# Kernel optimization log

Measured on AMD Instinct MI355X. Metric: run time of the kernel, lower is better.

The kernel has to match this reference:

```python
import math
import jax, jax.numpy as jnp
import numpy as np

NUM_FILTERS = 4
MAX_RADIUS = 0.999
B, L = 32, 524288


def setup_inputs() -> dict:
    key = jax.random.key(0)
    kx, kr, ka, kb1, kb2 = jax.random.split(key, 5)
    return {
        "x": jax.random.normal(kx, (B, L), dtype=jnp.float32),
        "log_radius": jax.random.normal(kr, (NUM_FILTERS,), dtype=jnp.float32),
        "raw_angle": jax.random.normal(ka, (NUM_FILTERS,), dtype=jnp.float32),
        "b0": jnp.ones((NUM_FILTERS,), dtype=jnp.float32),
        "b1": 0.1 * jax.random.normal(kb1, (NUM_FILTERS,), dtype=jnp.float32),
        "b2": 0.1 * jax.random.normal(kb2, (NUM_FILTERS,), dtype=jnp.float32),
    }


def _apply_single_biquad(x, b0, b1, b2, a1, a2):
    # Direct Form II Transposed, sequential over time via lax.scan.
    # x: (B, L); scalars b0,b1,b2,a1,a2.
    Bv = x.shape[0]
    s0 = (jnp.zeros((Bv,), x.dtype), jnp.zeros((Bv,), x.dtype))

    def step(carry, xn):
        s1, s2 = carry
        yn = b0 * xn + s1
        s1n = b1 * xn - a1 * yn + s2
        s2n = b2 * xn - a2 * yn
        return (s1n, s2n), yn

    _, ys = jax.lax.scan(step, s0, x.T)  # ys: (L, B)
    return ys.T


def reference(x, log_radius, raw_angle, b0, b1, b2):
    # Stable pole parameterization: radius in (0, MAX_RADIUS), angle in (0, pi)
    radius = jax.nn.sigmoid(log_radius) * MAX_RADIUS
    angle = jax.nn.sigmoid(raw_angle) * math.pi
    a1 = -2.0 * radius * jnp.cos(angle)  # (F,)
    a2 = radius * radius                 # (F,)
    y = x
    for f in range(NUM_FILTERS):  # cascade (series) application
        y = _apply_single_biquad(y, b0[f], b1[f], b2[f], a1[f], a2[f])
    return y
```

## Files before the change

kernel.cpp:

```cpp
#include <hip/hip_runtime.h>
#include <math.h>

#define Bn 32
#define Ln 524288
#define NF 4

#define TPB   256
#define NW    (TPB / 64)
#define CPT   18
#define OUT   4096
#define WU    512
#define S_WG  (OUT + WU)
#define TPR   (Ln / OUT)
#define NTILE 2
#define NT    (Bn * TPR / NTILE)

#define SLOT4  (S_WG / 4)
#define OSLOT4 (OUT / 4)
#define WSLOT4 (WU / 4)

#define COEF_OFF 0
#define POWJ_OFF 64
#define XW1_OFF  448
#define PLM4_OFF 512
#define WSEQ_OFF 3072

#define WAGG_L (SLOT4 * 4)
#define LDS_F  (WAGG_L + 32)

__device__ __forceinline__ constexpr int prow(int p) {
    return (p < 2) ? 0 : (p < 4) ? 1 : (p < 8) ? 2 : (p < 12) ? 3
         : (p < 18) ? 4 : (p < 24) ? 5 : (p < 32) ? 6 : 7;
}
__device__ __forceinline__ constexpr int pcol(int p) {
    return p - ((p < 2) ? 0 : (p < 4) ? 2 : (p < 8) ? 4 : (p < 12) ? 8
              : (p < 18) ? 12 : (p < 24) ? 18 : (p < 32) ? 24 : 32);
}

__global__ void precompute_k(const float* __restrict__ lr,
                             const float* __restrict__ ra,
                             const float* __restrict__ b0,
                             const float* __restrict__ b1,
                             const float* __restrict__ b2,
                             float* __restrict__ ws) {
    __shared__ double A2d[6][64];
    __shared__ float  A2f[6][64];
    __shared__ double Tw[64];
    const int t = threadIdx.x;

    if (t < NF) {
        double r   = 0.999 / (1.0 + exp(-(double)lr[t]));
        double ang = 3.14159265358979323846 / (1.0 + exp(-(double)ra[t]));
        ws[COEF_OFF + t * 5 + 0] = b0[t];
        ws[COEF_OFF + t * 5 + 1] = b1[t];
        ws[COEF_OFF + t * 5 + 2] = b2[t];
        ws[COEF_OFF + t * 5 + 3] = (float)(-2.0 * r * cos(ang));
        ws[COEF_OFF + t * 5 + 4] = (float)(r * r);
    }
    __syncthreads();

    if (t < 8) {
        double cb0[NF], cb1[NF], cb2[NF], ca1[NF], ca2[NF];
        for (int f = 0; f < NF; ++f) {
            cb0[f] = (double)ws[COEF_OFF + f * 5 + 0];
            cb1[f] = (double)ws[COEF_OFF + f * 5 + 1];
            cb2[f] = (double)ws[COEF_OFF + f * 5 + 2];
            ca1[f] = (double)ws[COEF_OFF + f * 5 + 3];
            ca2[f] = (double)ws[COEF_OFF + f * 5 + 4];
        }
        double s[8];
        for (int r = 0; r < 8; ++r) s[r] = 0.0;
        s[t] = 1.0;
        for (int n = 0; n < CPT; ++n) {
            double v = 0.0;
            for (int f = 0; f < NF; ++f) {
                double y     = cb0[f] * v + s[2 * f];
                s[2 * f]     = cb1[f] * v - ca1[f] * y + s[2 * f + 1];
                s[2 * f + 1] = cb2[f] * v - ca2[f] * y;
                v = y;
            }
            ws[WSEQ_OFF + n * 8 + t] = (float)v;
        }
        for (int r = 0; r < 8; ++r) A2d[0][r * 8 + t] = s[r];
    }
    __syncthreads();

    A2f[0][t] = (float)A2d[0][t];
    ws[POWJ_OFF + t] = A2f[0][t];
    const int r8 = t >> 3, c8 = t & 7;
    for (int j = 1; j <= 6; ++j) {
        const double* S = A2d[j - 1];
        double acc = 0.0;
        for (int m = 0; m < 8; ++m) acc += S[r8 * 8 + m] * S[m * 8 + c8];
        Tw[t] = acc;
        __syncthreads();
        if (j <= 5) {
            A2d[j][t] = Tw[t];
            A2f[j][t] = (float)Tw[t];
            ws[POWJ_OFF + j * 64 + t] = (float)Tw[t];
        } else {
            ws[XW1_OFF + t] = (float)Tw[t];
        }
        __syncthreads();
    }

    float M[64];
#pragma unroll
    for (int i = 0; i < 64; ++i) M[i] = ((i >> 3) == (i & 7)) ? 1.f : 0.f;
    for (int j = 0; j < 6; ++j) {
        if ((t >> j) & 1) {
            float Tn[64];
            for (int r = 0; r < 8; ++r)
                for (int c = 0; c < 8; ++c) {
                    float acc = 0.f;
                    for (int m = 0; m < 8; ++m)
                        acc = fmaf(M[r * 8 + m], A2f[j][m * 8 + c], acc);
                    Tn[r * 8 + c] = acc;
                }
            for (int i = 0; i < 64; ++i) M[i] = Tn[i];
        }
    }
    for (int p = 0; p < 40; ++p)
        ws[PLM4_OFF + (p >> 2) * 256 + t * 4 + (p & 3)] = M[prow(p) * 8 + pcol(p)];
}

__device__ __forceinline__ void step1(float& u, float* s,
                                      const float* c0, const float* c1,
                                      const float* c2, const float* A1,
                                      const float* A2) {
#pragma unroll
    for (int f = 0; f < NF; ++f) {
        float yv     = fmaf(c0[f], u, s[2 * f]);
        s[2 * f]     = fmaf(-A1[f], yv, fmaf(c1[f], u, s[2 * f + 1]));
        s[2 * f + 1] = fmaf(-A2[f], yv, c2[f] * u);
        u = yv;
    }
}

__device__ __forceinline__ void matvec_acc_sp(float* o, const float* __restrict__ T,
                                              const float* p) {
#pragma unroll
    for (int r = 0; r < 8; ++r) {
        const int ncol = (r | 1) + 1;
#pragma unroll
        for (int c = 0; c < 8; ++c)
            if (c < ncol) o[r] = fmaf(T[r * 8 + c], p[c], o[r]);
    }
}
__device__ __forceinline__ void matvec_rep_sp(float* h, const float* __restrict__ T) {
    float tmp[8];
#pragma unroll
    for (int r = 0; r < 8; ++r) {
        const int ncol = (r | 1) + 1;
        float acc = 0.f;
#pragma unroll
        for (int c = 0; c < 8; ++c)
            if (c < ncol) acc = fmaf(T[r * 8 + c], h[c], acc);
        tmp[r] = acc;
    }
#pragma unroll
    for (int r = 0; r < 8; ++r) h[r] = tmp[r];
}

__global__ __launch_bounds__(TPB, 8) void biquad_k(const float* __restrict__ x,
                                                   const float* __restrict__ ws,
                                                   float* __restrict__ y) {
    __shared__ __align__(16) float ldsf[LDS_F];
    float4* lds4 = (float4*)ldsf;
    float2* lds2 = (float2*)ldsf;
    const int t    = threadIdx.x;
    const int lane = t & 63;
    const int w    = t >> 6;

    const float* __restrict__ mats = ws + POWJ_OFF;
    const float* __restrict__ xw1  = ws + XW1_OFF;
    const float4* xg4 = (const float4*)x;
    float4* yg4 = (float4*)y;

    float c0[NF], c1[NF], c2[NF], A1[NF], A2[NF];
#pragma unroll
    for (int f = 0; f < NF; ++f) {
        c0[f] = ws[COEF_OFF + f * 5 + 0];
        c1[f] = ws[COEF_OFF + f * 5 + 1];
        c2[f] = ws[COEF_OFF + f * 5 + 2];
        A1[f] = ws[COEF_OFF + f * 5 + 3];
        A2[f] = ws[COEF_OFF + f * 5 + 4];
    }

    float4 pf[5];
    {
        const int tile = blockIdx.x * NTILE;
        const int tpos = tile % TPR;
        const long base4 = (long)(tile / TPR) * (Ln / 4) + (long)tpos * OSLOT4 - WSLOT4;
#pragma unroll
        for (int j = 0; j < 5; ++j) {
            const int n4 = j * TPB + t;
            pf[j] = make_float4(0.f, 0.f, 0.f, 0.f);
            if (n4 < SLOT4 && (tpos > 0 || n4 >= WSLOT4)) pf[j] = xg4[base4 + n4];
        }
    }

#pragma unroll
    for (int k = 0; k < NTILE; ++k) {
        const int tile = blockIdx.x * NTILE + k;
        const int row  = tile / TPR;
        const int tpos = tile % TPR;

        if (k > 0) __syncthreads();

#pragma unroll
        for (int j = 0; j < 5; ++j) {
            const int n4 = j * TPB + t;
            if (n4 < SLOT4) lds4[n4] = pf[j];
        }
        __syncthreads();

        if (k + 1 < NTILE) {
            const int ntile = tile + 1;
            const int ntpos = ntile % TPR;
            const long nbase4 = (long)(ntile / TPR) * (Ln / 4) + (long)ntpos * OSLOT4 - WSLOT4;
#pragma unroll
            for (int j = 0; j < 5; ++j) {
                const int n4 = j * TPB + t;
                float4 v = make_float4(0.f, 0.f, 0.f, 0.f);
                if (n4 < SLOT4 && (ntpos > 0 || n4 >= WSLOT4)) v = xg4[nbase4 + n4];
                pf[j] = v;
            }
        }

        float s[8];
#pragma unroll
        for (int r = 0; r < 8; ++r) s[r] = 0.f;
        {
            float2 xr[CPT / 2];
#pragma unroll
            for (int i = 0; i < CPT / 2; ++i) xr[i] = lds2[(CPT / 2) * t + i];
#pragma unroll
            for (int i = 0; i < CPT / 2; ++i) {
                float u;
                u = xr[i].x; step1(u, s, c0, c1, c2, A1, A2); xr[i].x = u;
                u = xr[i].y; step1(u, s, c0, c1, c2, A1, A2); xr[i].y = u;
            }
#pragma unroll
            for (int i = 0; i < CPT / 2; ++i) lds2[(CPT / 2) * t + i] = xr[i];
        }

        float v8[8];
#pragma unroll
        for (int r = 0; r < 8; ++r) v8[r] = s[r];
#pragma unroll
        for (int j = 0; j < 6; ++j) {
            const int st = 1 << j;
            float p[8];
#pragma unroll
            for (int r = 0; r < 8; ++r) p[r] = __shfl_up(v8[r], st, 64);
            if (lane >= st) matvec_acc_sp(v8, mats + j * 64, p);
        }

        if (lane == 63) {
#pragma unroll
            for (int r = 0; r < 8; ++r) ldsf[WAGG_L + w * 8 + r] = v8[r];
        }
        __syncthreads();

        float H[8];
#pragma unroll
        for (int r = 0; r < 8; ++r) H[r] = 0.f;
#pragma unroll
        for (int m = 0; m < NW - 1; ++m) {
            if (m < w) {
                matvec_rep_sp(H, xw1);
#pragma unroll
                for (int r = 0; r < 8; ++r) H[r] += ldsf[WAGG_L + m * 8 + r];
            }
        }

        float dlt[8];
#pragma unroll
        for (int r = 0; r < 8; ++r) dlt[r] = 0.f;
        {
            const float4* plm4 = (const float4*)(ws + PLM4_OFF);
#pragma unroll
            for (int g = 0; g < 10; ++g) {
                const float4 mv = plm4[g * 64 + lane];
                dlt[prow(4 * g + 0)] = fmaf(mv.x, H[pcol(4 * g + 0)], dlt[prow(4 * g + 0)]);
                dlt[prow(4 * g + 1)] = fmaf(mv.y, H[pcol(4 * g + 1)], dlt[prow(4 * g + 1)]);
                dlt[prow(4 * g + 2)] = fmaf(mv.z, H[pcol(4 * g + 2)], dlt[prow(4 * g + 2)]);
                dlt[prow(4 * g + 3)] = fmaf(mv.w, H[pcol(4 * g + 3)], dlt[prow(4 * g + 3)]);
            }
        }
#pragma unroll
        for (int r = 0; r < 8; ++r) {
            const float pv = __shfl_up(v8[r], 1, 64);
            if (lane > 0) dlt[r] += pv;
        }

        const float* __restrict__ wsq = ws + WSEQ_OFF;
#pragma unroll
        for (int i = 0; i < CPT / 2; ++i) {
            float2 v = lds2[(CPT / 2) * t + i];
            float a0 = 0.f, a1 = 0.f;
#pragma unroll
            for (int kk = 0; kk < 8; ++kk) {
                a0 = fmaf(wsq[(2 * i) * 8 + kk], dlt[kk], a0);
                a1 = fmaf(wsq[(2 * i + 1) * 8 + kk], dlt[kk], a1);
            }
            v.x += a0;
            v.y += a1;
            lds2[(CPT / 2) * t + i] = v;
        }
        __syncthreads();

        const long obase4 = (long)row * (Ln / 4) + (long)tpos * OSLOT4;
#pragma unroll
        for (int j = 0; j < 4; ++j) {
            const int n4 = WSLOT4 + j * TPB + t;
            yg4[obase4 + (n4 - WSLOT4)] = lds4[n4];
        }
    }
}

extern "C" void kernel_launch(void* const* d_in, const int* in_sizes, int n_in,
                              void* d_out, int out_size, void* d_ws, size_t ws_size,
                              hipStream_t stream) {
    const float* x  = (const float*)d_in[0];
    const float* lr = (const float*)d_in[1];
    const float* ra = (const float*)d_in[2];
    const float* b0 = (const float*)d_in[3];
    const float* b1 = (const float*)d_in[4];
    const float* b2 = (const float*)d_in[5];
    float* y  = (float*)d_out;
    float* ws = (float*)d_ws;

    precompute_k<<<dim3(1), dim3(64), 0, stream>>>(lr, ra, b0, b1, b2, ws);
    biquad_k<<<dim3(NT), dim3(TPB), 0, stream>>>(x, ws, y);
}
```

Measured before the change: 56.99 us.

## Double-buffer input tiles in LDS via direct global-to-LDS loads

```diff
diff --git a/kernel.cpp b/kernel.cpp
--- a/kernel.cpp
+++ b/kernel.cpp
@@ -12,8 +12,8 @@
 #define WU    512
 #define S_WG  (OUT + WU)
 #define TPR   (Ln / OUT)
-#define NTILE 2
-#define NT    (Bn * TPR / NTILE)
+#define NTILE 4
+#define NWG   (Bn * TPR / NTILE)
 
 #define SLOT4  (S_WG / 4)
 #define OSLOT4 (OUT / 4)
@@ -24,9 +24,6 @@
 #define XW1_OFF  448
 #define PLM4_OFF 512
 #define WSEQ_OFF 3072
-
-#define WAGG_L (SLOT4 * 4)
-#define LDS_F  (WAGG_L + 32)
 
 __device__ __forceinline__ constexpr int prow(int p) {
     return (p < 2) ? 0 : (p < 4) ? 1 : (p < 8) ? 2 : (p < 12) ? 3
@@ -162,20 +159,35 @@
     for (int r = 0; r < 8; ++r) h[r] = tmp[r];
 }
 
-__global__ __launch_bounds__(TPB, 8) void biquad_k(const float* __restrict__ x,
+__device__ __forceinline__ void dma16(const float4* g, float4* l) {
+    __builtin_amdgcn_global_load_lds(
+        (const __attribute__((address_space(1))) unsigned int*)g,
+        (__attribute__((address_space(3))) unsigned int*)l,
+        16, 0, 0);
+}
+
+#define BAR_LGKM() do { asm volatile("s_waitcnt lgkmcnt(0)" ::: "memory"); \
+                        __builtin_amdgcn_s_barrier(); } while (0)
+
+__global__ __launch_bounds__(TPB, 4) void biquad_k(const float* __restrict__ x,
                                                    const float* __restrict__ ws,
                                                    float* __restrict__ y) {
-    __shared__ __align__(16) float ldsf[LDS_F];
-    float4* lds4 = (float4*)ldsf;
-    float2* lds2 = (float2*)ldsf;
+    __shared__ __align__(16) float4 buf[2][SLOT4];
+    __shared__ float wagg[NW * 8];
     const int t    = threadIdx.x;
     const int lane = t & 63;
     const int w    = t >> 6;
 
+    const float4* xg4 = (const float4*)x;
+    float4* yg4 = (float4*)y;
+
+    const int g0   = blockIdx.x * NTILE;
+    const int row  = g0 / TPR;
+    const int tp0  = g0 % TPR;
+    const long rowbase = (long)row * (Ln / 4);
+
     const float* __restrict__ mats = ws + POWJ_OFF;
     const float* __restrict__ xw1  = ws + XW1_OFF;
-    const float4* xg4 = (const float4*)x;
-    float4* yg4 = (float4*)y;
 
     float c0[NF], c1[NF], c2[NF], A1[NF], A2[NF];
 #pragma unroll
@@ -187,46 +199,42 @@
         A2[f] = ws[COEF_OFF + f * 5 + 4];
     }
 
-    float4 pf[5];
     {
-        const int tile = blockIdx.x * NTILE;
-        const int tpos = tile % TPR;
-        const long base4 = (long)(tile / TPR) * (Ln / 4) + (long)tpos * OSLOT4 - WSLOT4;
-#pragma unroll
-        for (int j = 0; j < 5; ++j) {
+        const bool skipwu = (tp0 == 0);
+        const long base4 = rowbase + (long)tp0 * OSLOT4 - WSLOT4;
+        if (skipwu && t < WSLOT4) buf[0][t] = make_float4(0.f, 0.f, 0.f, 0.f);
+#pragma unroll
+        for (int j = 0; j < 4; ++j) {
             const int n4 = j * TPB + t;
-            pf[j] = make_float4(0.f, 0.f, 0.f, 0.f);
-            if (n4 < SLOT4 && (tpos > 0 || n4 >= WSLOT4)) pf[j] = xg4[base4 + n4];
-        }
-    }
-
-#pragma unroll
+            if (!skipwu || n4 >= WSLOT4) dma16(xg4 + base4 + n4, &buf[0][n4]);
+        }
+        if (t < SLOT4 - 4 * TPB) {
+            const int n4 = 4 * TPB + t;
+            dma16(xg4 + base4 + n4, &buf[0][n4]);
+        }
+    }
+    asm volatile("s_waitcnt vmcnt(0)" ::: "memory");
+    BAR_LGKM();
+
     for (int k = 0; k < NTILE; ++k) {
-        const int tile = blockIdx.x * NTILE + k;
-        const int row  = tile / TPR;
-        const int tpos = tile % TPR;
-
-        if (k > 0) __syncthreads();
-
-#pragma unroll
-        for (int j = 0; j < 5; ++j) {
-            const int n4 = j * TPB + t;
-            if (n4 < SLOT4) lds4[n4] = pf[j];
-        }
-        __syncthreads();
+        const int cur  = k & 1;
+        const int tpos = tp0 + k;
 
         if (k + 1 < NTILE) {
-            const int ntile = tile + 1;
-            const int ntpos = ntile % TPR;
-            const long nbase4 = (long)(ntile / TPR) * (Ln / 4) + (long)ntpos * OSLOT4 - WSLOT4;
-#pragma unroll
-            for (int j = 0; j < 5; ++j) {
+            const long nb4 = rowbase + (long)(tpos + 1) * OSLOT4 - WSLOT4;
+            float4* dst = &buf[cur ^ 1][0];
+#pragma unroll
+            for (int j = 0; j < 4; ++j) {
                 const int n4 = j * TPB + t;
-                float4 v = make_float4(0.f, 0.f, 0.f, 0.f);
-                if (n4 < SLOT4 && (ntpos > 0 || n4 >= WSLOT4)) v = xg4[nbase4 + n4];
-                pf[j] = v;
-            }
-        }
+                dma16(xg4 + nb4 + n4, dst + n4);
+            }
+            if (t < SLOT4 - 4 * TPB) {
+                const int n4 = 4 * TPB + t;
+                dma16(xg4 + nb4 + n4, dst + n4);
+            }
+        }
+
+        float2* l2 = (float2*)&buf[cur][0];
 
         float s[8];
 #pragma unroll
@@ -234,7 +242,7 @@
         {
             float2 xr[CPT / 2];
 #pragma unroll
-            for (int i = 0; i < CPT / 2; ++i) xr[i] = lds2[(CPT / 2) * t + i];
+            for (int i = 0; i < CPT / 2; ++i) xr[i] = l2[(CPT / 2) * t + i];
 #pragma unroll
             for (int i = 0; i < CPT / 2; ++i) {
                 float u;
@@ -242,7 +250,7 @@
                 u = xr[i].y; step1(u, s, c0, c1, c2, A1, A2); xr[i].y = u;
             }
 #pragma unroll
-            for (int i = 0; i < CPT / 2; ++i) lds2[(CPT / 2) * t + i] = xr[i];
+            for (int i = 0; i < CPT / 2; ++i) l2[(CPT / 2) * t + i] = xr[i];
         }
 
         float v8[8];
@@ -259,9 +267,9 @@
 
         if (lane == 63) {
 #pragma unroll
-            for (int r = 0; r < 8; ++r) ldsf[WAGG_L + w * 8 + r] = v8[r];
-        }
-        __syncthreads();
+            for (int r = 0; r < 8; ++r) wagg[w * 8 + r] = v8[r];
+        }
+        BAR_LGKM();
 
         float H[8];
 #pragma unroll
@@ -271,7 +279,7 @@
             if (m < w) {
                 matvec_rep_sp(H, xw1);
 #pragma unroll
-                for (int r = 0; r < 8; ++r) H[r] += ldsf[WAGG_L + m * 8 + r];
+                for (int r = 0; r < 8; ++r) H[r] += wagg[m * 8 + r];
             }
         }
 
@@ -298,7 +306,7 @@
         const float* __restrict__ wsq = ws + WSEQ_OFF;
 #pragma unroll
         for (int i = 0; i < CPT / 2; ++i) {
-            float2 v = lds2[(CPT / 2) * t + i];
+            float2 v = l2[(CPT / 2) * t + i];
             float a0 = 0.f, a1 = 0.f;
 #pragma unroll
             for (int kk = 0; kk < 8; ++kk) {
@@ -307,15 +315,20 @@
             }
             v.x += a0;
             v.y += a1;
-            lds2[(CPT / 2) * t + i] = v;
-        }
-        __syncthreads();
-
-        const long obase4 = (long)row * (Ln / 4) + (long)tpos * OSLOT4;
+            l2[(CPT / 2) * t + i] = v;
+        }
+        BAR_LGKM();
+
+        const long obase4 = rowbase + (long)tpos * OSLOT4;
 #pragma unroll
         for (int j = 0; j < 4; ++j) {
             const int n4 = WSLOT4 + j * TPB + t;
-            yg4[obase4 + (n4 - WSLOT4)] = lds4[n4];
+            yg4[obase4 + (n4 - WSLOT4)] = buf[cur][n4];
+        }
+
+        if (k + 1 < NTILE) {
+            asm volatile("s_waitcnt vmcnt(4)" ::: "memory");
+            __builtin_amdgcn_s_barrier();
         }
     }
 }
@@ -333,5 +346,5 @@
     float* ws = (float*)d_ws;
 
     precompute_k<<<dim3(1), dim3(64), 0, stream>>>(lr, ra, b0, b1, b2, ws);
-    biquad_k<<<dim3(NT), dim3(TPB), 0, stream>>>(x, ws, y);
-}
+    biquad_k<<<dim3(NWG), dim3(TPB), 0, stream>>>(x, ws, y);
+}
```

Result: slower. 64.35 us (+12.9%).
